# Optimization experiments

Hardware: AMD Instinct MI355X
Metric: run time of the kernel (lower is better)

Reference implementation:

```python
import jax, jax.numpy as jnp
import numpy as np

HIDDEN = 1024
BETA = 1.0
SPARSITY_THRESHOLD = 1.0


def _sparsemax(x):
    # Faithful port of the module's custom sparsemax (including its
    # nonstandard per-position tau). Operates over the last axis.
    n = x.shape[-1]
    z = x - jnp.max(x, axis=-1, keepdims=True)
    sum_z = jnp.sum(z, axis=-1, keepdims=True)
    step = (sum_z - 1.0) / n                       # step_size
    sorted_z = -jnp.sort(-z, axis=-1)              # descending sort
    cumsum_z = jnp.cumsum(sorted_z, axis=-1)
    is_gt = sorted_z > step
    rng = jnp.arange(1, n + 1, dtype=jnp.int32)
    k = jnp.max(rng * is_gt, axis=-1, keepdims=True).astype(x.dtype)
    tau = (cumsum_z - 1.0 - step * k) / k          # [.., n] per-position tau
    return jnp.clip(z - tau, 0.0)


def setup_inputs() -> dict:
    key = jax.random.key(0)
    kx, kq, kk, kv = jax.random.split(key, 4)
    B, S, D = 4, 2048, 1024
    x = jax.random.normal(kx, (B, S, D), dtype=jnp.float32)
    # torch Linear weight layout: [out_features, in_features]
    scale = 1.0 / np.sqrt(D)
    Wq = jax.random.normal(kq, (HIDDEN, D), dtype=jnp.float32) * scale
    Wk = jax.random.normal(kk, (HIDDEN, D), dtype=jnp.float32) * scale
    Wv = jax.random.normal(kv, (HIDDEN, D), dtype=jnp.float32) * scale
    return {"x": x, "Wq": Wq, "Wk": Wk, "Wv": Wv}


def reference(x, Wq, Wk, Wv):
    Q = jnp.einsum('bsd,hd->bsh', x, Wq)
    K = jnp.einsum('bsd,hd->bsh', x, Wk)
    V = jnp.einsum('bsd,hd->bsh', x, Wv)
    energy = jnp.einsum('bsh,bth->bst', Q, K) / jnp.sqrt(jnp.asarray(HIDDEN, x.dtype))
    scores = energy * BETA
    sparsity = jnp.mean(jnp.abs(x))
    attention = jax.lax.cond(
        sparsity < SPARSITY_THRESHOLD,
        _sparsemax,
        lambda s: jax.nn.softmax(s, axis=-1),
        scores,
    )
    return jnp.einsum('bst,bth->bsh', attention, V)
```

## Files before the change

### kernel.cpp

```cpp
#include <hip/hip_runtime.h>
#include <math.h>

#define B_   4
#define S_   2048
#define D_   1024
#define H_   1024
#define NROW 2048
#define TOTX 8388608.0f

typedef _Float16 f16x8 __attribute__((ext_vector_type(8)));
typedef float f32x4 __attribute__((ext_vector_type(4)));

__device__ __forceinline__ unsigned short f2h(float f) {
  _Float16 h = (_Float16)f;
  return __builtin_bit_cast(unsigned short, h);
}

#define GLD16(gp, lp)                                                            \
  __builtin_amdgcn_global_load_lds(                                              \
      (__attribute__((address_space(1))) void*)(gp),                             \
      (__attribute__((address_space(3))) void*)(lp), 16, 0, 0)

__global__ __launch_bounds__(256) void f2h_abs_kernel(const float* __restrict__ in,
                                                      unsigned short* __restrict__ out,
                                                      float* absOut, int n4) {
  int i0 = blockIdx.x * 256 + threadIdx.x;
  int stride = gridDim.x * 256;
  float s = 0.f;
  for (int i = i0; i < n4; i += stride) {
    float4 v = ((const float4*)in)[i];
    ushort4 o;
    o.x = f2h(v.x); o.y = f2h(v.y); o.z = f2h(v.z); o.w = f2h(v.w);
    ((ushort4*)out)[i] = o;
    s += fabsf(v.x) + fabsf(v.y) + fabsf(v.z) + fabsf(v.w);
  }
#pragma unroll
  for (int off = 32; off; off >>= 1) s += __shfl_xor(s, off);
  __shared__ float red[4];
  if ((threadIdx.x & 63) == 0) red[threadIdx.x >> 6] = s;
  __syncthreads();
  if (threadIdx.x == 0) atomicAdd(absOut, red[0] + red[1] + red[2] + red[3]);
}

__global__ __launch_bounds__(256) void f2h3_kernel(const float* __restrict__ a,
                                                   const float* __restrict__ b,
                                                   const float* __restrict__ c,
                                                   unsigned short* __restrict__ oa,
                                                   unsigned short* __restrict__ ob,
                                                   unsigned short* __restrict__ oc,
                                                   int n4) {
  int i = blockIdx.x * 256 + threadIdx.x;
  if (i >= n4) return;
  const float* in = (blockIdx.y == 0) ? a : (blockIdx.y == 1) ? b : c;
  unsigned short* out = (blockIdx.y == 0) ? oa : (blockIdx.y == 1) ? ob : oc;
  float4 v = ((const float4*)in)[i];
  ushort4 o;
  o.x = f2h(v.x); o.y = f2h(v.y); o.z = f2h(v.z); o.w = f2h(v.w);
  ((ushort4*)out)[i] = o;
}

template <int MI, bool OUT_F16>
__global__ __launch_bounds__(512, 2) void gemm8_nt(const unsigned short* __restrict__ A,
                                                   const unsigned short* __restrict__ B,
                                                   void* __restrict__ Cv,
                                                   unsigned short* __restrict__ VT,
                                                   int M, int N, int K,
                                                   long long sA, long long sB, long long sC,
                                                   float scale) {
  constexpr int BM  = MI * 32;
  constexpr int ASZ = BM * 32;
  constexpr int BSZ = 256 * 32;
  constexpr int TSZ = ASZ + BSZ;
  constexpr int MH  = MI / 2;

  const int bz = blockIdx.z;
  A += (long long)bz * sA;
  B += (long long)bz * sB;

  __shared__ __align__(16) unsigned short lds[2 * TSZ];

  const int tid = threadIdx.x;
  const int lane = tid & 63;
  const int w = tid >> 6;
  const int wr = w >> 2;
  const int wc = w & 3;
  const int m0 = blockIdx.y * BM, n0 = blockIdx.x * 256;

  f32x4 acc[MI][4] = {};

  const int srow = tid >> 2;
  const int scol = ((lane & 3) ^ ((lane >> 3) & 3)) * 8;
  const unsigned short* gA0 = A + (long long)(m0 + srow) * K + scol;
  const unsigned short* gA1 = gA0 + (long long)128 * K;
  const unsigned short* gB0 = B + (long long)(n0 + srow) * K + scol;
  const unsigned short* gB1 = gB0 + (long long)128 * K;
  const int wb = w * 512;

  const int fm = lane & 15;
  const int col8 = ((lane >> 4) ^ ((lane >> 1) & 3)) * 8;
  int aoff[MI], boff[4];
#pragma unroll
  for (int mi = 0; mi < MI; ++mi) aoff[mi] = (wr * (MI * 16) + mi * 16 + fm) * 32 + col8;
#pragma unroll
  for (int ni = 0; ni < 4; ++ni) boff[ni] = ASZ + (wc * 64 + ni * 16 + fm) * 32 + col8;

  const int nt = K >> 5;

#define STAGE(nb, k0)                                    \
  do {                                                   \
    unsigned short* L_ = lds + (nb) * TSZ;               \
    GLD16(gA0 + (k0), L_ + wb);                          \
    if (MI == 8) GLD16(gA1 + (k0), L_ + 4096 + wb);      \
    GLD16(gB0 + (k0), L_ + ASZ + wb);                    \
    GLD16(gB1 + (k0), L_ + ASZ + 4096 + wb);             \
  } while (0)

  STAGE(0, 0);
  STAGE(1, 32);
  if (MI == 8) asm volatile("s_waitcnt vmcnt(4)" ::: "memory");
  else         asm volatile("s_waitcnt vmcnt(3)" ::: "memory");
  __builtin_amdgcn_s_barrier();

  for (int t = 0; t < nt; ++t) {
    const unsigned short* L = lds + (t & 1) * TSZ;
    f16x8 af[MH], bf[4];
#pragma unroll
    for (int mi = 0; mi < MH; ++mi) af[mi] = *(const f16x8*)(L + aoff[mi]);
#pragma unroll
    for (int ni = 0; ni < 4; ++ni) bf[ni] = *(const f16x8*)(L + boff[ni]);
    __builtin_amdgcn_s_setprio(1);
#pragma unroll
    for (int mi = 0; mi < MH; ++mi)
#pragma unroll
      for (int ni = 0; ni < 4; ++ni)
        acc[mi][ni] = __builtin_amdgcn_mfma_f32_16x16x32_f16(af[mi], bf[ni],
                                                             acc[mi][ni], 0, 0, 0);
    __builtin_amdgcn_s_setprio(0);
    f16x8 ag[MH];
#pragma unroll
    for (int mi = 0; mi < MH; ++mi) ag[mi] = *(const f16x8*)(L + aoff[MH + mi]);
    asm volatile("s_waitcnt lgkmcnt(0)" ::: "memory");
    __builtin_amdgcn_sched_barrier(0);
    __builtin_amdgcn_s_barrier();
    if (t + 2 < nt) STAGE(t & 1, (t + 2) << 5);
    __builtin_amdgcn_s_setprio(1);
#pragma unroll
    for (int mi = 0; mi < MH; ++mi)
#pragma unroll
      for (int ni = 0; ni < 4; ++ni)
        acc[MH + mi][ni] = __builtin_amdgcn_mfma_f32_16x16x32_f16(ag[mi], bf[ni],
                                                                  acc[MH + mi][ni], 0, 0, 0);
    __builtin_amdgcn_s_setprio(0);
    if (t + 2 < nt) {
      if (MI == 8) asm volatile("s_waitcnt vmcnt(4)" ::: "memory");
      else         asm volatile("s_waitcnt vmcnt(3)" ::: "memory");
    } else if (t + 1 < nt) {
      asm volatile("s_waitcnt vmcnt(0)" ::: "memory");
    }
    __builtin_amdgcn_s_barrier();
  }
#undef STAGE

  const int cm = (lane >> 4) * 4;
  const int cn = lane & 15;
  if (VT != nullptr && bz == 2) {
#pragma unroll
    for (int mi = 0; mi < MI; ++mi)
#pragma unroll
      for (int ni = 0; ni < 4; ++ni) {
        int m = m0 + wr * (MI * 16) + mi * 16 + cm;
        int n = n0 + wc * 64 + ni * 16 + cn;
        int b = m >> 11, s = m & 2047;
        ushort4 o;
        o.x = f2h(acc[mi][ni][0] * scale);
        o.y = f2h(acc[mi][ni][1] * scale);
        o.z = f2h(acc[mi][ni][2] * scale);
        o.w = f2h(acc[mi][ni][3] * scale);
        *(ushort4*)(VT + (long long)b * (H_ * S_) + (long long)n * S_ + s) = o;
      }
    return;
  }
#pragma unroll
  for (int mi = 0; mi < MI; ++mi)
#pragma unroll
    for (int ni = 0; ni < 4; ++ni) {
#pragma unroll
      for (int r = 0; r < 4; ++r) {
        long long m = m0 + wr * (MI * 16) + mi * 16 + cm + r;
        long long n = n0 + wc * 64 + ni * 16 + cn;
        float v = acc[mi][ni][r] * scale;
        if (OUT_F16)
          ((unsigned short*)Cv)[(long long)bz * sC + m * N + n] = f2h(v);
        else
          ((float*)Cv)[(long long)bz * sC + m * N + n] = v;
      }
    }
}

template <int K, int J>
__device__ __forceinline__ void intra_s(float (&r)[32]) {
#pragma unroll
  for (int v = 0; v < 32; ++v)
    if ((v & J) == 0) {
      const int u = v | J;
      const bool dsc = ((v & K) == 0);
      float a = r[v], b = r[u];
      float mx = fmaxf(a, b), mn = fminf(a, b);
      r[v] = dsc ? mx : mn;
      r[u] = dsc ? mn : mx;
    }
}

template <int J>
__device__ __forceinline__ void intra_desc(float (&r)[32]) {
#pragma unroll
  for (int v = 0; v < 32; ++v)
    if ((v & J) == 0) {
      const int u = v | J;
      float a = r[v], b = r[u];
      r[v] = fmaxf(a, b);
      r[u] = fminf(a, b);
    }
}

template <int JL>
__device__ __forceinline__ void cross_desc(float (&r)[32], int lane, int bp32) {
  const bool keepmax = ((lane & JL) == 0);
  float b[32];
#pragma unroll
  for (int v = 0; v < 32; ++v) {
    int av = __builtin_bit_cast(int, r[v]);
    int bv;
    if constexpr (JL == 32)
      bv = __builtin_amdgcn_ds_bpermute(bp32, av);
    else
      bv = __builtin_amdgcn_ds_swizzle(av, (JL << 10) | 0x1F);
    b[v] = __builtin_bit_cast(float, bv);
  }
  __builtin_amdgcn_sched_barrier(0);
#pragma unroll
  for (int v = 0; v < 32; ++v) {
    float mx = fmaxf(r[v], b[v]), mn = fminf(r[v], b[v]);
    r[v] = keepmax ? mx : mn;
  }
}

__device__ __forceinline__ void signfix(float (&r)[32], unsigned fix) {
#pragma unroll
  for (int v = 0; v < 32; ++v)
    r[v] = __builtin_bit_cast(float, __builtin_bit_cast(unsigned, r[v]) ^ fix);
}

__global__ __launch_bounds__(256, 4) void attn_row_wave(const float* __restrict__ scores,
                                                        unsigned short* __restrict__ attn,
                                                        const float* __restrict__ absSum) {
  const int tid = threadIdx.x;
  const int lane = tid & 63;
  const int row = blockIdx.x * 4 + (tid >> 6);
  const float* rowp = scores + (long long)row * NROW;
  unsigned short* aout = attn + (long long)row * NROW;
  const int bp32 = (lane ^ 32) << 2;

  const float4* rp4 = (const float4*)rowp + lane * 8;
  float r[32];
  float lm = -INFINITY, lsraw = 0.f;
#pragma unroll
  for (int q = 0; q < 8; ++q) {
    float4 v = rp4[q];
    r[q * 4 + 0] = v.x; r[q * 4 + 1] = v.y;
    r[q * 4 + 2] = v.z; r[q * 4 + 3] = v.w;
    lm = fmaxf(lm, fmaxf(fmaxf(v.x, v.y), fmaxf(v.z, v.w)));
    lsraw += v.x + v.y + v.z + v.w;
  }
#pragma unroll
  for (int off = 32; off; off >>= 1) {
    lm = fmaxf(lm, __shfl_xor(lm, off, 64));
    lsraw += __shfl_xor(lsraw, off, 64);
  }

  const bool use_softmax = (absSum[0] * (1.0f / TOTX)) >= 1.0f;

  if (use_softmax) {
    float ls = 0.f;
#pragma unroll
    for (int v = 0; v < 32; ++v) { r[v] = expf(r[v] - lm); ls += r[v]; }
#pragma unroll
    for (int off = 32; off; off >>= 1) ls += __shfl_xor(ls, off, 64);
    float inv = 1.0f / ls;
    ushort4* op = (ushort4*)(aout + lane * 32);
#pragma unroll
    for (int q = 0; q < 8; ++q) {
      ushort4 o;
      o.x = f2h(r[q * 4 + 0] * inv); o.y = f2h(r[q * 4 + 1] * inv);
      o.z = f2h(r[q * 4 + 2] * inv); o.w = f2h(r[q * 4 + 3] * inv);
      op[q] = o;
    }
    return;
  }

#pragma unroll
  for (int v = 0; v < 32; ++v) r[v] -= lm;
  const float step = ((lsraw - (float)NROW * lm) - 1.0f) * (1.0f / (float)NROW);

  intra_s<2, 1>(r);
  intra_s<4, 2>(r); intra_s<4, 1>(r);
  intra_s<8, 4>(r); intra_s<8, 2>(r); intra_s<8, 1>(r);
  intra_s<16, 8>(r); intra_s<16, 4>(r); intra_s<16, 2>(r); intra_s<16, 1>(r);

  unsigned cur = (unsigned)(lane & 1) << 31;
  signfix(r, cur);
  intra_desc<16>(r); intra_desc<8>(r); intra_desc<4>(r);
  intra_desc<2>(r); intra_desc<1>(r);

  { unsigned want = (unsigned)(lane & 2) << 30;
    signfix(r, cur ^ want); cur = want; }
  cross_desc<1>(r, lane, bp32);
  intra_desc<16>(r); intra_desc<8>(r); intra_desc<4>(r);
  intra_desc<2>(r); intra_desc<1>(r);

  { unsigned want = (unsigned)(lane & 4) << 29;
    signfix(r, cur ^ want); cur = want; }
  cross_desc<2>(r, lane, bp32); cross_desc<1>(r, lane, bp32);
  intra_desc<16>(r); intra_desc<8>(r); intra_desc<4>(r);
  intra_desc<2>(r); intra_desc<1>(r);

  { unsigned want = (unsigned)(lane & 8) << 28;
    signfix(r, cur ^ want); cur = want; }
  cross_desc<4>(r, lane, bp32); cross_desc<2>(r, lane, bp32);
  cross_desc<1>(r, lane, bp32);
  intra_desc<16>(r); intra_desc<8>(r); intra_desc<4>(r);
  intra_desc<2>(r); intra_desc<1>(r);

  { unsigned want = (unsigned)(lane & 16) << 27;
    signfix(r, cur ^ want); cur = want; }
  cross_desc<8>(r, lane, bp32); cross_desc<4>(r, lane, bp32);
  cross_desc<2>(r, lane, bp32); cross_desc<1>(r, lane, bp32);
  intra_desc<16>(r); intra_desc<8>(r); intra_desc<4>(r);
  intra_desc<2>(r); intra_desc<1>(r);

  { unsigned want = (unsigned)(lane & 32) << 26;
    signfix(r, cur ^ want); cur = want; }
  cross_desc<16>(r, lane, bp32); cross_desc<8>(r, lane, bp32);
  cross_desc<4>(r, lane, bp32); cross_desc<2>(r, lane, bp32);
  cross_desc<1>(r, lane, bp32);
  intra_desc<16>(r); intra_desc<8>(r); intra_desc<4>(r);
  intra_desc<2>(r); intra_desc<1>(r);

  signfix(r, cur);
  cross_desc<32>(r, lane, bp32); cross_desc<16>(r, lane, bp32);
  cross_desc<8>(r, lane, bp32); cross_desc<4>(r, lane, bp32);
  cross_desc<2>(r, lane, bp32); cross_desc<1>(r, lane, bp32);
  intra_desc<16>(r); intra_desc<8>(r); intra_desc<4>(r);
  intra_desc<2>(r); intra_desc<1>(r);

  float lcnt = 0.f;
#pragma unroll
  for (int v = 0; v < 32; ++v) lcnt += (r[v] > step) ? 1.0f : 0.0f;
#pragma unroll
  for (int off = 32; off; off >>= 1) lcnt += __shfl_xor(lcnt, off, 64);
  const float kf = lcnt;

  float run = 0.f;
#pragma unroll
  for (int v = 0; v < 32; ++v) { run += r[v]; r[v] = run; }
  float pre = run;
#pragma unroll
  for (int off = 1; off < 64; off <<= 1) {
    float t = __shfl_up(pre, off, 64);
    if (lane >= off) pre += t;
  }
  pre -= run;
#pragma unroll
  for (int v = 0; v < 32; ++v) r[v] += pre;

  const float inv_k = 1.0f / kf;
  const float c1 = 1.0f + step * kf;

  unsigned long long up = (unsigned long long)rowp;
  asm volatile("" : "+v"(up));
  const float4* rp4e = (const float4*)up + lane * 8;
  ushort4* op = (ushort4*)(aout + lane * 32);
#pragma unroll
  for (int q = 0; q < 8; ++q) {
    float4 v = rp4e[q];
    ushort4 o;
    o.x = f2h(fmaxf((v.x - lm) - (r[q * 4 + 0] - c1) * inv_k, 0.0f));
    o.y = f2h(fmaxf((v.y - lm) - (r[q * 4 + 1] - c1) * inv_k, 0.0f));
    o.z = f2h(fmaxf((v.z - lm) - (r[q * 4 + 2] - c1) * inv_k, 0.0f));
    o.w = f2h(fmaxf((v.w - lm) - (r[q * 4 + 3] - c1) * inv_k, 0.0f));
    op[q] = o;
  }
}

extern "C" void kernel_launch(void* const* d_in, const int* in_sizes, int n_in,
                              void* d_out, int out_size, void* d_ws, size_t ws_size,
                              hipStream_t stream) {
  const float* x  = (const float*)d_in[0];
  const float* Wq = (const float*)d_in[1];
  const float* Wk = (const float*)d_in[2];
  const float* Wv = (const float*)d_in[3];
  float* out = (float*)d_out;

  const long long NX = (long long)B_ * S_ * D_;
  const long long NW = (long long)H_ * D_;

  char* base = (char*)d_ws;
  unsigned short* x16  = (unsigned short*)(base);
  unsigned short* Wq16 = (unsigned short*)(base + (16ll << 20));
  unsigned short* Wk16 = (unsigned short*)(base + (18ll << 20));
  unsigned short* Wv16 = (unsigned short*)(base + (20ll << 20));
  float*          Sc   = (float*)(base);
  unsigned short* Vt16 = (unsigned short*)(base + (64ll << 20));
  unsigned short* Q16  = (unsigned short*)(base + (80ll << 20));
  unsigned short* K16  = (unsigned short*)(base + (96ll << 20));
  unsigned short* A16  = (unsigned short*)(base + (80ll << 20));
  float*          flag = (float*)(base + (144ll << 20));

  hipMemsetAsync(flag, 0, sizeof(float), stream);

  f2h_abs_kernel<<<1024, 256, 0, stream>>>(x, x16, flag, (int)(NX / 4));
  f2h3_kernel<<<dim3((int)(NW / 4 + 255) / 256, 3), 256, 0, stream>>>(
      Wq, Wk, Wv, Wq16, Wk16, Wv16, (int)(NW / 4));

  {
    dim3 grid(H_ / 256, (B_ * S_) / 128, 3);
    gemm8_nt<4, true><<<grid, 512, 0, stream>>>(x16, Wq16, Q16, Vt16,
                                                B_ * S_, H_, D_,
                                                0, (long long)NW, (long long)(8ll << 20),
                                                1.0f);
  }

  {
    dim3 grid(S_ / 256, S_ / 128, B_);
    gemm8_nt<4, false><<<grid, 512, 0, stream>>>(Q16, K16, Sc, nullptr,
                                                 S_, S_, H_,
                                                 (long long)S_ * H_, (long long)S_ * H_,
                                                 (long long)S_ * S_, 1.0f / 32.0f);
  }

  attn_row_wave<<<(B_ * S_) / 4, 256, 0, stream>>>(Sc, A16, flag);

  {
    dim3 grid(H_ / 256, S_ / 128, B_);
    gemm8_nt<4, false><<<grid, 512, 0, stream>>>(A16, Vt16, out, nullptr,
                                                 S_, H_, S_,
                                                 (long long)S_ * S_, (long long)H_ * S_,
                                                 (long long)S_ * H_, 1.0f);
  }
}
```

Measured before the change: 335.8 us.

## Use triple-buffered GEMM pipeline and store scores as fp16

The GEMM main loop moves from a double-buffered scheme, with a mid-iteration barrier and split MFMA halves, to a three-buffer rotation. The next stage's global-to-LDS loads are issued before the MFMAs, leaving one barrier per k-step. Separately, the QK^T scores are written as fp16 instead of fp32, and the sparsemax/softmax row kernel reads fp16 with 8-wide vector loads, halving score traffic. This raises LDS use per block, which may lower occupancy, and fp16 scores lose precision before the sort and cumsum.

```diff
diff --git a/kernel.cpp b/kernel.cpp
--- a/kernel.cpp
+++ b/kernel.cpp
@@ -10,10 +10,14 @@
 
 typedef _Float16 f16x8 __attribute__((ext_vector_type(8)));
 typedef float f32x4 __attribute__((ext_vector_type(4)));
+typedef unsigned short us8 __attribute__((ext_vector_type(8)));
 
 __device__ __forceinline__ unsigned short f2h(float f) {
   _Float16 h = (_Float16)f;
   return __builtin_bit_cast(unsigned short, h);
+}
+__device__ __forceinline__ float h2f(unsigned short u) {
+  return (float)__builtin_bit_cast(_Float16, u);
 }
 
 #define GLD16(gp, lp)                                                            \
@@ -71,13 +75,12 @@
   constexpr int ASZ = BM * 32;
   constexpr int BSZ = 256 * 32;
   constexpr int TSZ = ASZ + BSZ;
-  constexpr int MH  = MI / 2;
 
   const int bz = blockIdx.z;
   A += (long long)bz * sA;
   B += (long long)bz * sB;
 
-  __shared__ __align__(16) unsigned short lds[2 * TSZ];
+  __shared__ __align__(16) unsigned short lds[3 * TSZ];
 
   const int tid = threadIdx.x;
   const int lane = tid & 63;
@@ -106,50 +109,40 @@
 
   const int nt = K >> 5;
 
-#define STAGE(nb, k0)                                    \
+#define STAGEP(Lp, k0)                                   \
   do {                                                   \
-    unsigned short* L_ = lds + (nb) * TSZ;               \
-    GLD16(gA0 + (k0), L_ + wb);                          \
-    if (MI == 8) GLD16(gA1 + (k0), L_ + 4096 + wb);      \
-    GLD16(gB0 + (k0), L_ + ASZ + wb);                    \
-    GLD16(gB1 + (k0), L_ + ASZ + 4096 + wb);             \
+    GLD16(gA0 + (k0), (Lp) + wb);                        \
+    if (MI == 8) GLD16(gA1 + (k0), (Lp) + 4096 + wb);    \
+    GLD16(gB0 + (k0), (Lp) + ASZ + wb);                  \
+    GLD16(gB1 + (k0), (Lp) + ASZ + 4096 + wb);           \
   } while (0)
 
-  STAGE(0, 0);
-  STAGE(1, 32);
+  unsigned short* L0 = lds;
+  unsigned short* L1 = lds + TSZ;
+  unsigned short* L2 = lds + 2 * TSZ;
+
+  STAGEP(L0, 0);
+  STAGEP(L1, 32);
   if (MI == 8) asm volatile("s_waitcnt vmcnt(4)" ::: "memory");
   else         asm volatile("s_waitcnt vmcnt(3)" ::: "memory");
   __builtin_amdgcn_s_barrier();
 
   for (int t = 0; t < nt; ++t) {
-    const unsigned short* L = lds + (t & 1) * TSZ;
-    f16x8 af[MH], bf[4];
-#pragma unroll
-    for (int mi = 0; mi < MH; ++mi) af[mi] = *(const f16x8*)(L + aoff[mi]);
-#pragma unroll
-    for (int ni = 0; ni < 4; ++ni) bf[ni] = *(const f16x8*)(L + boff[ni]);
+    f16x8 af[MI], bf[4];
+#pragma unroll
+    for (int mi = 0; mi < MI; ++mi) af[mi] = *(const f16x8*)(L0 + aoff[mi]);
+#pragma unroll
+    for (int ni = 0; ni < 4; ++ni) bf[ni] = *(const f16x8*)(L0 + boff[ni]);
+    if (t + 2 < nt) STAGEP(L2, (t + 2) << 5);
+    asm volatile("s_waitcnt lgkmcnt(0)" ::: "memory");
+    __builtin_amdgcn_sched_barrier(0);
     __builtin_amdgcn_s_setprio(1);
 #pragma unroll
-    for (int mi = 0; mi < MH; ++mi)
+    for (int mi = 0; mi < MI; ++mi)
 #pragma unroll
       for (int ni = 0; ni < 4; ++ni)
         acc[mi][ni] = __builtin_amdgcn_mfma_f32_16x16x32_f16(af[mi], bf[ni],
                                                              acc[mi][ni], 0, 0, 0);
-    __builtin_amdgcn_s_setprio(0);
-    f16x8 ag[MH];
-#pragma unroll
-    for (int mi = 0; mi < MH; ++mi) ag[mi] = *(const f16x8*)(L + aoff[MH + mi]);
-    asm volatile("s_waitcnt lgkmcnt(0)" ::: "memory");
-    __builtin_amdgcn_sched_barrier(0);
-    __builtin_amdgcn_s_barrier();
-    if (t + 2 < nt) STAGE(t & 1, (t + 2) << 5);
-    __builtin_amdgcn_s_setprio(1);
-#pragma unroll
-    for (int mi = 0; mi < MH; ++mi)
-#pragma unroll
-      for (int ni = 0; ni < 4; ++ni)
-        acc[MH + mi][ni] = __builtin_amdgcn_mfma_f32_16x16x32_f16(ag[mi], bf[ni],
-                                                                  acc[MH + mi][ni], 0, 0, 0);
     __builtin_amdgcn_s_setprio(0);
     if (t + 2 < nt) {
       if (MI == 8) asm volatile("s_waitcnt vmcnt(4)" ::: "memory");
@@ -158,8 +151,9 @@
       asm volatile("s_waitcnt vmcnt(0)" ::: "memory");
     }
     __builtin_amdgcn_s_barrier();
-  }
-#undef STAGE
+    unsigned short* tmp = L0; L0 = L1; L1 = L2; L2 = tmp;
+  }
+#undef STAGEP
 
   const int cm = (lane >> 4) * 4;
   const int cn = lane & 15;
@@ -251,26 +245,29 @@
     r[v] = __builtin_bit_cast(float, __builtin_bit_cast(unsigned, r[v]) ^ fix);
 }
 
-__global__ __launch_bounds__(256, 4) void attn_row_wave(const float* __restrict__ scores,
+__global__ __launch_bounds__(256, 4) void attn_row_wave(const unsigned short* __restrict__ scores,
                                                         unsigned short* __restrict__ attn,
                                                         const float* __restrict__ absSum) {
   const int tid = threadIdx.x;
   const int lane = tid & 63;
   const int row = blockIdx.x * 4 + (tid >> 6);
-  const float* rowp = scores + (long long)row * NROW;
+  const unsigned short* rowp = scores + (long long)row * NROW;
   unsigned short* aout = attn + (long long)row * NROW;
   const int bp32 = (lane ^ 32) << 2;
 
-  const float4* rp4 = (const float4*)rowp + lane * 8;
+  const us8* rp = (const us8*)(rowp + lane * 32);
   float r[32];
   float lm = -INFINITY, lsraw = 0.f;
 #pragma unroll
-  for (int q = 0; q < 8; ++q) {
-    float4 v = rp4[q];
-    r[q * 4 + 0] = v.x; r[q * 4 + 1] = v.y;
-    r[q * 4 + 2] = v.z; r[q * 4 + 3] = v.w;
-    lm = fmaxf(lm, fmaxf(fmaxf(v.x, v.y), fmaxf(v.z, v.w)));
-    lsraw += v.x + v.y + v.z + v.w;
+  for (int q = 0; q < 4; ++q) {
+    us8 h = rp[q];
+#pragma unroll
+    for (int j = 0; j < 8; ++j) {
+      float f = h2f((unsigned short)h[j]);
+      r[q * 8 + j] = f;
+      lm = fmaxf(lm, f);
+      lsraw += f;
+    }
   }
 #pragma unroll
   for (int off = 32; off; off >>= 1) {
@@ -287,12 +284,12 @@
 #pragma unroll
     for (int off = 32; off; off >>= 1) ls += __shfl_xor(ls, off, 64);
     float inv = 1.0f / ls;
-    ushort4* op = (ushort4*)(aout + lane * 32);
-#pragma unroll
-    for (int q = 0; q < 8; ++q) {
-      ushort4 o;
-      o.x = f2h(r[q * 4 + 0] * inv); o.y = f2h(r[q * 4 + 1] * inv);
-      o.z = f2h(r[q * 4 + 2] * inv); o.w = f2h(r[q * 4 + 3] * inv);
+    us8* op = (us8*)(aout + lane * 32);
+#pragma unroll
+    for (int q = 0; q < 4; ++q) {
+      us8 o;
+#pragma unroll
+      for (int j = 0; j < 8; ++j) o[j] = f2h(r[q * 8 + j] * inv);
       op[q] = o;
     }
     return;
@@ -378,16 +375,17 @@
 
   unsigned long long up = (unsigned long long)rowp;
   asm volatile("" : "+v"(up));
-  const float4* rp4e = (const float4*)up + lane * 8;
-  ushort4* op = (ushort4*)(aout + lane * 32);
-#pragma unroll
-  for (int q = 0; q < 8; ++q) {
-    float4 v = rp4e[q];
-    ushort4 o;
-    o.x = f2h(fmaxf((v.x - lm) - (r[q * 4 + 0] - c1) * inv_k, 0.0f));
-    o.y = f2h(fmaxf((v.y - lm) - (r[q * 4 + 1] - c1) * inv_k, 0.0f));
-    o.z = f2h(fmaxf((v.z - lm) - (r[q * 4 + 2] - c1) * inv_k, 0.0f));
-    o.w = f2h(fmaxf((v.w - lm) - (r[q * 4 + 3] - c1) * inv_k, 0.0f));
+  const us8* rpe = (const us8*)up + lane * 4;
+  us8* op = (us8*)(aout + lane * 32);
+#pragma unroll
+  for (int q = 0; q < 4; ++q) {
+    us8 h = rpe[q];
+    us8 o;
+#pragma unroll
+    for (int j = 0; j < 8; ++j) {
+      float z = h2f((unsigned short)h[j]) - lm;
+      o[j] = f2h(fmaxf(z - (r[q * 8 + j] - c1) * inv_k, 0.0f));
+    }
     op[q] = o;
   }
 }
@@ -409,7 +407,7 @@
   unsigned short* Wq16 = (unsigned short*)(base + (16ll << 20));
   unsigned short* Wk16 = (unsigned short*)(base + (18ll << 20));
   unsigned short* Wv16 = (unsigned short*)(base + (20ll << 20));
-  float*          Sc   = (float*)(base);
+  unsigned short* Sc16 = (unsigned short*)(base);
   unsigned short* Vt16 = (unsigned short*)(base + (64ll << 20));
   unsigned short* Q16  = (unsigned short*)(base + (80ll << 20));
   unsigned short* K16  = (unsigned short*)(base + (96ll << 20));
@@ -432,13 +430,13 @@
 
   {
     dim3 grid(S_ / 256, S_ / 128, B_);
-    gemm8_nt<4, false><<<grid, 512, 0, stream>>>(Q16, K16, Sc, nullptr,
-                                                 S_, S_, H_,
-                                                 (long long)S_ * H_, (long long)S_ * H_,
-                                                 (long long)S_ * S_, 1.0f / 32.0f);
-  }
-
-  attn_row_wave<<<(B_ * S_) / 4, 256, 0, stream>>>(Sc, A16, flag);
+    gemm8_nt<4, true><<<grid, 512, 0, stream>>>(Q16, K16, Sc16, nullptr,
+                                                S_, S_, H_,
+                                                (long long)S_ * H_, (long long)S_ * H_,
+                                                (long long)S_ * S_, 1.0f / 32.0f);
+  }
+
+  attn_row_wave<<<(B_ * S_) / 4, 256, 0, stream>>>(Sc16, A16, flag);
 
   {
     dim3 grid(H_ / 256, S_ / 128, B_);
```

Result: faster. 314.3 us (-6.4%).
